# Kernel tuning notes

Hardware: AMD Instinct MI355X
Metric: run time of the kernel (lower is better)

Reference implementation:

```python
import jax, jax.numpy as jnp
import numpy as np

B, A, S, T, DE, D3 = 8, 32, 16, 750, 25, 58
L, DZ = 4, 512
KL_P = 0.0002


def setup_inputs() -> dict:
    key = jax.random.key(0)
    ks = jax.random.split(key, 6)
    return {
        "gt_emotion": jax.random.normal(ks[0], (B * A, T, DE), jnp.float32),
        "gt_3dmm": jax.random.normal(ks[1], (B * A, T, D3), jnp.float32),
        "pred_emotion": jax.random.normal(ks[2], (B * S, T, DE), jnp.float32),
        "pred_3dmm": jax.random.normal(ks[3], (B * S, T, D3), jnp.float32),
        "dist_mu": jax.random.normal(ks[4], (L, B * S, DZ), jnp.float32),
        "dist_scale": jax.random.uniform(ks[5], (L, B * S, DZ), jnp.float32, 0.5, 1.5),
        "num_appropriate": jnp.full((B,), A, jnp.int32),
        "num_samples": jnp.full((B,), S, jnp.int32),
    }


def reference(gt_emotion, gt_3dmm, pred_emotion, pred_3dmm, dist_mu, dist_scale,
              num_appropriate, num_samples):
    b = num_appropriate.shape[0]
    a = gt_emotion.shape[0] // b      # appropriate reactions per batch element
    s = pred_emotion.shape[0] // b    # predicted samples per batch element
    t, de = gt_emotion.shape[1], gt_emotion.shape[2]
    d3 = gt_3dmm.shape[2]

    ge = gt_emotion.reshape(b, a, t, de)
    g3 = gt_3dmm.reshape(b, a, t, d3)
    pe = pred_emotion.reshape(b, s, t, de)
    p3 = pred_3dmm.reshape(b, s, t, d3)

    # pairwise mean-MSE cost between every pred sample and every appropriate gt
    ce = jnp.mean((pe[:, :, None] - ge[:, None]) ** 2, axis=(3, 4))                    # [b,s,a]
    c1 = jnp.mean((p3[:, :, None, :, :52] - g3[:, None, :, :, :52]) ** 2, axis=(3, 4))
    c2 = jnp.mean((p3[:, :, None, :, 52:] - g3[:, None, :, :, 52:]) ** 2, axis=(3, 4))
    cost = ce + c1 + 10.0 * c2

    idx = jnp.argmin(cost, axis=2)                     # [b,s] best-match index (torch.no_grad)
    bidx = jnp.arange(b)[:, None]
    ge_sel = ge[bidx, idx]                             # [b,s,t,de] gathered gt
    g3_sel = g3[bidx, idx]                             # [b,s,t,d3]

    rec_loss = (jnp.mean((pe - ge_sel) ** 2)
                + jnp.mean((p3[..., :52] - g3_sel[..., :52]) ** 2)
                + 10.0 * jnp.mean((p3[..., 52:] - g3_sel[..., 52:]) ** 2))

    # KL(N(mu, scale) || N(0, 1)), mean per layer then averaged over layers
    kl = -jnp.log(dist_scale) + 0.5 * (dist_scale ** 2 + dist_mu ** 2 - 1.0)
    kld_loss = jnp.mean(kl)

    loss = rec_loss + KL_P * kld_loss
    return (loss, rec_loss, kld_loss)
```

## Files before the change

### kernel.cpp

```cpp
#include <hip/hip_runtime.h>

#define NB 8
#define NA 32
#define NS 16
#define KE 18750
#define K3 43500
#define ND3 58
#define NKL 262144

#define POS_PER_B 8
#define SE_SLABS 10
#define S3_SLABS 22
#define SLABS 32
#define CH_E 1876
#define CH_3 1978
#define COST_BLOCKS (NB * POS_PER_B * SLABS)
#define KL_BLOCKS 64
#define KL_PER_THR (NKL / (KL_BLOCKS * 256))

#define SW_E  0.0073029674f
#define SW_1  0.0050637127f
#define SW_2  0.0471404521f

__global__ __launch_bounds__(256, 4) void fused_kernel(
    const float* __restrict__ ge, const float* __restrict__ g3,
    const float* __restrict__ pe, const float* __restrict__ p3,
    const float* __restrict__ mu, const float* __restrict__ sc,
    float* __restrict__ cost, float* __restrict__ klsum)
{
    const int blk = blockIdx.x;
    const int tid = threadIdx.x;
    __shared__ float red[4][64];

    if (blk >= COST_BLOCKS) {
        const int kb = blk - COST_BLOCKS;
        float ks = 0.f;
        #pragma unroll
        for (int it = 0; it < KL_PER_THR; ++it) {
            const int i = kb * (256 * KL_PER_THR) + it * 256 + tid;
            const float m = mu[i], sg = sc[i];
            ks += 0.5f * (sg * sg + m * m - 1.0f) - logf(sg);
        }
        #pragma unroll
        for (int o = 32; o > 0; o >>= 1) ks += __shfl_xor(ks, o);
        const int lane = tid & 63, w = tid >> 6;
        if (lane == 0) red[0][w] = ks;
        __syncthreads();
        if (tid == 0)
            atomicAdd(klsum, red[0][0] + red[0][1] + red[0][2] + red[0][3]);
        return;
    }

    const int b    = blk >> 8;
    const int rem  = blk & 255;
    const int pos  = rem >> 5;
    const int slab = rem & 31;
    const int s0   = (pos >> 2) * 8;
    const int a0   = (pos & 3) * 8;

    const bool isE = slab < SE_SLABS;
    const int  KH  = (isE ? KE : K3) >> 1;
    const int  c0  = isE ? slab * CH_E : (slab - SE_SLABS) * CH_3;
    const int  kk0 = (c0 >> 1) + tid;
    const int  kkend = min((c0 + (isE ? CH_E : CH_3)) >> 1, KH);

    const float2* __restrict__ P = (const float2*)(isE ? pe + (size_t)(b * NS + s0) * KE
                                                       : p3 + (size_t)(b * NS + s0) * K3);
    const float2* __restrict__ G = (const float2*)(isE ? ge + (size_t)(b * NA + a0) * KE
                                                       : g3 + (size_t)(b * NA + a0) * K3);

    float acc[64];
    #pragma unroll
    for (int i = 0; i < 64; ++i) acc[i] = 0.f;

    if (isE) {
        for (int kk = kk0; kk < kkend; kk += 256) {
            float2 p[8], g[8];
            #pragma unroll
            for (int i = 0; i < 8; ++i) { p[i] = P[i * KH + kk]; }
            #pragma unroll
            for (int j = 0; j < 8; ++j) { g[j] = G[j * KH + kk]; }
            #pragma unroll
            for (int i = 0; i < 8; ++i) { p[i].x *= SW_E; p[i].y *= SW_E; }
            #pragma unroll
            for (int j = 0; j < 8; ++j) { g[j].x *= SW_E; g[j].y *= SW_E; }
            #pragma unroll
            for (int i = 0; i < 8; ++i)
                #pragma unroll
                for (int j = 0; j < 8; ++j) {
                    const float d0 = p[i].x - g[j].x;
                    const float d1 = p[i].y - g[j].y;
                    float t = fmaf(d0, d0, acc[i * 8 + j]);
                    acc[i * 8 + j] = fmaf(d1, d1, t);
                }
        }
    } else {
        int col = (2 * kk0) % ND3;
        for (int kk = kk0; kk < kkend; kk += 256) {
            const float sw = (col < 52) ? SW_1 : SW_2;
            col += 48; if (col >= ND3) col -= ND3;
            float2 p[8], g[8];
            #pragma unroll
            for (int i = 0; i < 8; ++i) { p[i] = P[i * KH + kk]; }
            #pragma unroll
            for (int j = 0; j < 8; ++j) { g[j] = G[j * KH + kk]; }
            #pragma unroll
            for (int i = 0; i < 8; ++i) { p[i].x *= sw; p[i].y *= sw; }
            #pragma unroll
            for (int j = 0; j < 8; ++j) { g[j].x *= sw; g[j].y *= sw; }
            #pragma unroll
            for (int i = 0; i < 8; ++i)
                #pragma unroll
                for (int j = 0; j < 8; ++j) {
                    const float d0 = p[i].x - g[j].x;
                    const float d1 = p[i].y - g[j].y;
                    float t = fmaf(d0, d0, acc[i * 8 + j]);
                    acc[i * 8 + j] = fmaf(d1, d1, t);
                }
        }
    }

    const int lane = tid & 63;
    int n = 64;
    #pragma unroll
    for (int step = 0; step < 6; ++step) {
        const int o = 1 << step;
        const bool hi = (lane & o) != 0;
        const int h = n >> 1;
        #pragma unroll
        for (int m = 0; m < h; ++m) {
            const float send = hi ? acc[m] : acc[m + h];
            const float recv = __shfl_xor(send, o);
            acc[m] = (hi ? acc[m + h] : acc[m]) + recv;
        }
        n = h;
    }

    const int w = tid >> 6;
    red[w][__brev((unsigned)lane) >> 26] = acc[0];
    __syncthreads();
    if (tid < 64) {
        const float v = red[0][tid] + red[1][tid] + red[2][tid] + red[3][tid];
        const int i = tid >> 3, j = tid & 7;
        atomicAdd(&cost[b * (NS * NA) + (s0 + i) * NA + (a0 + j)], v);
    }
}

__global__ __launch_bounds__(128) void finalize_kernel(
    const float* __restrict__ cost, const float* __restrict__ klsum,
    float* __restrict__ out)
{
    const int t = threadIdx.x;
    const float4* row = (const float4*)(cost + t * NA);
    float mn = 1e30f;
    #pragma unroll
    for (int q = 0; q < 8; ++q) {
        const float4 v = row[q];
        mn = fminf(mn, fminf(fminf(v.x, v.y), fminf(v.z, v.w)));
    }
    #pragma unroll
    for (int o = 32; o > 0; o >>= 1) mn += __shfl_xor(mn, o);
    __shared__ float r2[2];
    if ((t & 63) == 0) r2[t >> 6] = mn;
    __syncthreads();
    if (t == 0) {
        const float rec = (r2[0] + r2[1]) * (1.0f / (NB * NS));
        const float kld = klsum[0] * (1.0f / (float)NKL);
        out[0] = fmaf(0.0002f, kld, rec);
        out[1] = rec;
        out[2] = kld;
    }
}

extern "C" void kernel_launch(void* const* d_in, const int* in_sizes, int n_in,
                              void* d_out, int out_size, void* d_ws, size_t ws_size,
                              hipStream_t stream)
{
    const float* ge = (const float*)d_in[0];
    const float* g3 = (const float*)d_in[1];
    const float* pe = (const float*)d_in[2];
    const float* p3 = (const float*)d_in[3];
    const float* mu = (const float*)d_in[4];
    const float* sc = (const float*)d_in[5];

    float* cost  = (float*)d_ws;
    float* klsum = cost + NB * NS * NA;

    hipMemsetAsync(d_ws, 0, (NB * NS * NA + 1) * sizeof(float), stream);

    fused_kernel<<<COST_BLOCKS + KL_BLOCKS, 256, 0, stream>>>(
        ge, g3, pe, p3, mu, sc, cost, klsum);
    finalize_kernel<<<1, 128, 0, stream>>>(cost, klsum, (float*)d_out);
}
```

Before: 156.4 us.

## Expand squared distance into norms plus cross term and halve grid slabs

The pairwise weighted squared distance is rewritten as ||p||^2 + ||g||^2 - 2<p,g>. The inner loop now does one FMA per element pair instead of a subtract and an FMA. Per-row norms are accumulated separately in each block and reduced with atomics, and the finalize kernel rebuilds the cost from them. Slabs per tile drop from 32 to 16 with a fixed 8-trip unrolled loop, masked by zero weights, and launch bounds go to 3 waves. The expansion can lose precision through cancellation, which could change argmin choices on close ties.

```diff
diff --git a/kernel.cpp b/kernel.cpp
--- a/kernel.cpp
+++ b/kernel.cpp
@@ -5,16 +5,17 @@
 #define NS 16
 #define KE 18750
 #define K3 43500
+#define KH_E 9375
+#define KH_3 21750
 #define ND3 58
 #define NKL 262144
 
-#define POS_PER_B 8
-#define SE_SLABS 10
-#define S3_SLABS 22
-#define SLABS 32
-#define CH_E 1876
-#define CH_3 1978
-#define COST_BLOCKS (NB * POS_PER_B * SLABS)
+#define SE_SLABS 5
+#define SD_SLABS 11
+#define SLABS 16
+#define TRIPS 8
+#define CH2 2048
+#define COST_BLOCKS (NB * 8 * SLABS)
 #define KL_BLOCKS 64
 #define KL_PER_THR (NKL / (KL_BLOCKS * 256))
 
@@ -22,11 +23,12 @@
 #define SW_1  0.0050637127f
 #define SW_2  0.0471404521f
 
-__global__ __launch_bounds__(256, 4) void fused_kernel(
+__global__ __launch_bounds__(256, 3) void fused_kernel(
     const float* __restrict__ ge, const float* __restrict__ g3,
     const float* __restrict__ pe, const float* __restrict__ p3,
     const float* __restrict__ mu, const float* __restrict__ sc,
-    float* __restrict__ cost, float* __restrict__ klsum)
+    float* __restrict__ cross, float* __restrict__ normP,
+    float* __restrict__ normG, float* __restrict__ klsum)
 {
     const int blk = blockIdx.x;
     const int tid = threadIdx.x;
@@ -51,18 +53,18 @@
         return;
     }
 
-    const int b    = blk >> 8;
-    const int rem  = blk & 255;
-    const int pos  = rem >> 5;
-    const int slab = rem & 31;
-    const int s0   = (pos >> 2) * 8;
-    const int a0   = (pos & 3) * 8;
-
-    const bool isE = slab < SE_SLABS;
-    const int  KH  = (isE ? KE : K3) >> 1;
-    const int  c0  = isE ? slab * CH_E : (slab - SE_SLABS) * CH_3;
-    const int  kk0 = (c0 >> 1) + tid;
-    const int  kkend = min((c0 + (isE ? CH_E : CH_3)) >> 1, KH);
+    const int b     = blk >> 7;
+    const int rem   = blk & 127;
+    const int pos   = rem >> 4;
+    const int slab  = rem & 15;
+    const int stile = pos >> 2;
+    const int atile = pos & 3;
+    const int s0    = stile * 8;
+    const int a0    = atile * 8;
+
+    const bool isE  = slab < SE_SLABS;
+    const int  KH   = isE ? KH_E : KH_3;
+    const int  base = (isE ? slab : slab - SE_SLABS) * CH2;
 
     const float2* __restrict__ P = (const float2*)(isE ? pe + (size_t)(b * NS + s0) * KE
                                                        : p3 + (size_t)(b * NS + s0) * K3);
@@ -72,55 +74,77 @@
     float acc[64];
     #pragma unroll
     for (int i = 0; i < 64; ++i) acc[i] = 0.f;
-
-    if (isE) {
-        for (int kk = kk0; kk < kkend; kk += 256) {
-            float2 p[8], g[8];
+    float np[8], ng[8];
+    #pragma unroll
+    for (int i = 0; i < 8; ++i) { np[i] = 0.f; ng[i] = 0.f; }
+
+    int col = (2 * (base + tid)) % ND3;
+
+    #pragma unroll
+    for (int it = 0; it < TRIPS; ++it) {
+        const int  kk    = base + it * 256 + tid;
+        const bool valid = kk < KH;
+        const int  kc    = valid ? kk : (KH - 1);
+        float sw;
+        if (isE) {
+            sw = valid ? SW_E : 0.f;
+        } else {
+            sw = valid ? ((col < 52) ? SW_1 : SW_2) : 0.f;
+            col += 48; if (col >= ND3) col -= ND3;
+        }
+
+        float2 p[8], g[8];
+        #pragma unroll
+        for (int i = 0; i < 8; ++i) p[i] = P[i * KH + kc];
+        #pragma unroll
+        for (int j = 0; j < 8; ++j) g[j] = G[j * KH + kc];
+        #pragma unroll
+        for (int i = 0; i < 8; ++i) { p[i].x *= sw; p[i].y *= sw; }
+        #pragma unroll
+        for (int j = 0; j < 8; ++j) { g[j].x *= sw; g[j].y *= sw; }
+
+        #pragma unroll
+        for (int i = 0; i < 8; ++i)
+            np[i] = fmaf(p[i].y, p[i].y, fmaf(p[i].x, p[i].x, np[i]));
+        #pragma unroll
+        for (int j = 0; j < 8; ++j)
+            ng[j] = fmaf(g[j].y, g[j].y, fmaf(g[j].x, g[j].x, ng[j]));
+
+        #pragma unroll
+        for (int i = 0; i < 8; ++i)
             #pragma unroll
-            for (int i = 0; i < 8; ++i) { p[i] = P[i * KH + kk]; }
-            #pragma unroll
-            for (int j = 0; j < 8; ++j) { g[j] = G[j * KH + kk]; }
-            #pragma unroll
-            for (int i = 0; i < 8; ++i) { p[i].x *= SW_E; p[i].y *= SW_E; }
-            #pragma unroll
-            for (int j = 0; j < 8; ++j) { g[j].x *= SW_E; g[j].y *= SW_E; }
-            #pragma unroll
-            for (int i = 0; i < 8; ++i)
-                #pragma unroll
-                for (int j = 0; j < 8; ++j) {
-                    const float d0 = p[i].x - g[j].x;
-                    const float d1 = p[i].y - g[j].y;
-                    float t = fmaf(d0, d0, acc[i * 8 + j]);
-                    acc[i * 8 + j] = fmaf(d1, d1, t);
-                }
-        }
-    } else {
-        int col = (2 * kk0) % ND3;
-        for (int kk = kk0; kk < kkend; kk += 256) {
-            const float sw = (col < 52) ? SW_1 : SW_2;
-            col += 48; if (col >= ND3) col -= ND3;
-            float2 p[8], g[8];
-            #pragma unroll
-            for (int i = 0; i < 8; ++i) { p[i] = P[i * KH + kk]; }
-            #pragma unroll
-            for (int j = 0; j < 8; ++j) { g[j] = G[j * KH + kk]; }
-            #pragma unroll
-            for (int i = 0; i < 8; ++i) { p[i].x *= sw; p[i].y *= sw; }
-            #pragma unroll
-            for (int j = 0; j < 8; ++j) { g[j].x *= sw; g[j].y *= sw; }
-            #pragma unroll
-            for (int i = 0; i < 8; ++i)
-                #pragma unroll
-                for (int j = 0; j < 8; ++j) {
-                    const float d0 = p[i].x - g[j].x;
-                    const float d1 = p[i].y - g[j].y;
-                    float t = fmaf(d0, d0, acc[i * 8 + j]);
-                    acc[i * 8 + j] = fmaf(d1, d1, t);
-                }
-        }
+            for (int j = 0; j < 8; ++j) {
+                float t = fmaf(p[i].x, g[j].x, acc[i * 8 + j]);
+                acc[i * 8 + j] = fmaf(p[i].y, g[j].y, t);
+            }
     }
 
     const int lane = tid & 63;
+    const int w    = tid >> 6;
+
+    #pragma unroll
+    for (int i = 0; i < 8; ++i) {
+        #pragma unroll
+        for (int o = 32; o > 0; o >>= 1) {
+            np[i] += __shfl_xor(np[i], o);
+            ng[i] += __shfl_xor(ng[i], o);
+        }
+    }
+    if (lane == 0) {
+        #pragma unroll
+        for (int i = 0; i < 8; ++i) { red[w][i] = np[i]; red[w][8 + i] = ng[i]; }
+    }
+    __syncthreads();
+    if (tid < 8) {
+        const float v = red[0][tid] + red[1][tid] + red[2][tid] + red[3][tid];
+        atomicAdd(&normP[b * NS + s0 + tid], v * 0.25f);
+    } else if (tid < 16) {
+        const int j = tid - 8;
+        const float v = red[0][tid] + red[1][tid] + red[2][tid] + red[3][tid];
+        atomicAdd(&normG[b * NA + a0 + j], v * 0.5f);
+    }
+    __syncthreads();
+
     int n = 64;
     #pragma unroll
     for (int step = 0; step < 6; ++step) {
@@ -135,29 +159,30 @@
         }
         n = h;
     }
-
-    const int w = tid >> 6;
     red[w][__brev((unsigned)lane) >> 26] = acc[0];
     __syncthreads();
     if (tid < 64) {
         const float v = red[0][tid] + red[1][tid] + red[2][tid] + red[3][tid];
         const int i = tid >> 3, j = tid & 7;
-        atomicAdd(&cost[b * (NS * NA) + (s0 + i) * NA + (a0 + j)], v);
+        atomicAdd(&cross[(b * NS + s0 + i) * NA + (a0 + j)], v);
     }
 }
 
 __global__ __launch_bounds__(128) void finalize_kernel(
-    const float* __restrict__ cost, const float* __restrict__ klsum,
+    const float* __restrict__ cross, const float* __restrict__ normP,
+    const float* __restrict__ normG, const float* __restrict__ klsum,
     float* __restrict__ out)
 {
     const int t = threadIdx.x;
-    const float4* row = (const float4*)(cost + t * NA);
+    const int b = t >> 4;
+    const float npv = normP[t];
+    const float* cr = cross + t * NA;
+    const float* ngr = normG + b * NA;
     float mn = 1e30f;
     #pragma unroll
-    for (int q = 0; q < 8; ++q) {
-        const float4 v = row[q];
-        mn = fminf(mn, fminf(fminf(v.x, v.y), fminf(v.z, v.w)));
-    }
+    for (int a = 0; a < NA; ++a)
+        mn = fminf(mn, npv + ngr[a] - 2.0f * cr[a]);
+
     #pragma unroll
     for (int o = 32; o > 0; o >>= 1) mn += __shfl_xor(mn, o);
     __shared__ float r2[2];
@@ -183,12 +208,14 @@
     const float* mu = (const float*)d_in[4];
     const float* sc = (const float*)d_in[5];
 
-    float* cost  = (float*)d_ws;
-    float* klsum = cost + NB * NS * NA;
-
-    hipMemsetAsync(d_ws, 0, (NB * NS * NA + 1) * sizeof(float), stream);
+    float* cross = (float*)d_ws;
+    float* normP = cross + NB * NS * NA;
+    float* normG = normP + NB * NS;
+    float* klsum = normG + NB * NA;
+
+    hipMemsetAsync(d_ws, 0, (NB * NS * NA + NB * NS + NB * NA + 1) * sizeof(float), stream);
 
     fused_kernel<<<COST_BLOCKS + KL_BLOCKS, 256, 0, stream>>>(
-        ge, g3, pe, p3, mu, sc, cost, klsum);
-    finalize_kernel<<<1, 128, 0, stream>>>(cost, klsum, (float*)d_out);
+        ge, g3, pe, p3, mu, sc, cross, normP, normG, klsum);
+    finalize_kernel<<<1, 128, 0, stream>>>(cross, normP, normG, klsum, (float*)d_out);
 }
```

New measurement: 268.3 us. +71.5%, slower.
